# Kernel tuning notes

Hardware: AMD Instinct MI355X
Metric: run time of the kernel (lower is better)

## Reference

```python
import jax, jax.numpy as jnp
import numpy as np

K_NEIGH = 20
GROUPS = 4
KPTS = 9  # 3x3 deformable kernel
FH, FW = 240, 320


def _bn(x, p):
    # p: (4,C) rows = gamma, beta, running_mean, running_var ; x: (B,C,...)
    g, b, m, v = p[0], p[1], p[2], p[3]
    shp = (1, -1) + (1,) * (x.ndim - 2)
    return (x - m.reshape(shp)) * (g.reshape(shp) / jnp.sqrt(v.reshape(shp) + 1e-5)) + b.reshape(shp)


def _lrelu(x):
    return jnp.where(x >= 0, x, 0.2 * x)


def _c1x1(x, w):  # w: (Cout,Cin)
    return jnp.einsum('oc,bc...->bo...', w, x)


def _hswish(x):
    return x * jnp.clip(x + 3.0, 0.0, 6.0) / 6.0


def _coord_att(x, c1w, c1b, bnp, chw, chb, cww, cwb):
    B, C, H, W = x.shape
    ph = x.mean(axis=3, keepdims=True)                              # (B,C,H,1)
    pw = x.mean(axis=2, keepdims=True).transpose(0, 1, 3, 2)        # (B,C,W,1)
    y = jnp.concatenate([ph, pw], axis=2)                           # (B,C,H+W,1)
    y = _hswish(_bn(_c1x1(y, c1w) + c1b.reshape(1, -1, 1, 1), bnp))
    yh, yw = y[:, :, :H], y[:, :, H:]
    ah = jax.nn.sigmoid(_c1x1(yh, chw) + chb.reshape(1, -1, 1, 1))                         # (B,C,H,1)
    aw = jax.nn.sigmoid(_c1x1(yw.transpose(0, 1, 3, 2), cww) + cwb.reshape(1, -1, 1, 1))   # (B,C,1,W)
    return x * ah * aw


def _knn(x, k):
    xx = jnp.sum(x * x, axis=1)                     # (B,N)
    inner = jnp.einsum('bcn,bcm->bnm', x, x)
    pd = 2.0 * inner - xx[:, :, None] - xx[:, None, :]   # negative sq. distance
    return jax.lax.top_k(pd, k)[1]                  # (B,N,k)


def _graph_feature(x, k):
    B, C, N = x.shape
    idx = _knn(x, k)
    xt = x.transpose(0, 2, 1)                       # (B,N,C)
    nb = jax.vmap(lambda a, i: a[i])(xt, idx)       # (B,N,k,C)
    ctr = xt[:, :, None, :]
    f = jnp.concatenate([nb - ctr, jnp.broadcast_to(ctr, (B, N, k, C))], axis=3)
    return f.transpose(0, 3, 1, 2)                  # (B,2C,N,k)


def _dcnv4(x, off_w, off_b, val_w, val_b, out_w, out_b):
    B, C, H, W = x.shape
    Cg = C // GROUPS
    xh = x.transpose(0, 2, 3, 1)                    # (B,H,W,C)
    value = xh @ val_w + val_b
    om = (xh @ off_w + off_b).reshape(B, H, W, GROUPS, KPTS, 3)
    offs, mask = om[..., :2], om[..., 2]            # DCNv4: mask used un-normalized
    ky, kx = jnp.meshgrid(jnp.arange(-1, 2), jnp.arange(-1, 2), indexing='ij')
    kgrid = jnp.stack([kx.ravel(), ky.ravel()], -1).astype(x.dtype)      # (K,2) xy
    gy, gx = jnp.meshgrid(jnp.arange(H), jnp.arange(W), indexing='ij')
    base = jnp.stack([gx, gy], -1).astype(x.dtype)  # (H,W,2)
    loc = base[None, :, :, None, None, :] + kgrid + offs                 # (B,H,W,G,K,2)
    vflat = value.reshape(B, H * W, GROUPS, Cg)
    outs = []
    for g in range(GROUPS):
        lx = loc[:, :, :, g, :, 0]
        ly = loc[:, :, :, g, :, 1]                  # (B,H,W,K)
        x0 = jnp.floor(lx); y0 = jnp.floor(ly)
        wx = lx - x0; wy = ly - y0
        vg = vflat[:, :, g]                         # (B,HW,Cg)
        samp = jnp.zeros((B, H, W, KPTS, Cg), x.dtype)
        for yi, xi, w in ((y0, x0, (1 - wx) * (1 - wy)), (y0, x0 + 1, wx * (1 - wy)),
                          (y0 + 1, x0, (1 - wx) * wy), (y0 + 1, x0 + 1, wx * wy)):
            inb = (yi >= 0) & (yi < H) & (xi >= 0) & (xi < W)
            ii = (jnp.clip(yi, 0, H - 1) * W + jnp.clip(xi, 0, W - 1)).astype(jnp.int32)
            gathered = jax.vmap(lambda v, i: v[i])(vg, ii.reshape(B, -1)).reshape(B, H, W, KPTS, Cg)
            samp = samp + (w * inb)[..., None] * gathered
        outs.append(jnp.einsum('bhwk,bhwkc->bhwc', mask[:, :, :, g], samp))
    out = jnp.concatenate(outs, axis=-1) @ out_w + out_b
    return out.transpose(0, 3, 1, 2)


def setup_inputs() -> dict:
    key = jax.random.key(0)
    ks = jax.random.split(key, 24)
    B, N, IN_CH, FEAT_DIM = 2, 4096, 3, 128
    pc = jax.random.normal(ks[0], (B, 8, N), jnp.float32)
    v = jax.random.uniform(ks[1], (B, 1, N), jnp.float32, -240.0, 240.0)
    u = jax.random.uniform(ks[2], (B, 1, N), jnp.float32, -320.0, 320.0)
    pc = jnp.concatenate([v, u, pc[:, 2:]], axis=1)
    feat_s00 = jax.random.normal(ks[3], (B, IN_CH, 480, 640), jnp.float32)

    def w(k, shape, s=0.05):
        return jax.random.normal(k, shape, jnp.float32) * s

    def bn(c):
        return jnp.stack([jnp.ones(c), jnp.zeros(c), jnp.zeros(c), jnp.ones(c)]).astype(jnp.float32)

    OC = GROUPS * KPTS * 3
    return dict(
        pc_xyzrgb=pc, feat_s00=feat_s00,
        preconv_w=w(ks[4], (24, IN_CH, 3, 3)), preconv_b=jnp.zeros(24, jnp.float32),
        ca_c1_w=w(ks[5], (8, 24)), ca_c1_b=jnp.zeros(8, jnp.float32), ca_bn=bn(8),
        ca_ch_w=w(ks[6], (24, 8)), ca_ch_b=jnp.zeros(24, jnp.float32),
        ca_cw_w=w(ks[7], (24, 8)), ca_cw_b=jnp.zeros(24, jnp.float32),
        conv1_w=w(ks[8], (64, 64)), bn1=bn(64),
        conv2_w=w(ks[9], (64, 128)), bn2=bn(64),
        conv3_w=w(ks[10], (128, 128)), bn3=bn(128),
        lin4a_w=w(ks[11], (256, 256)), lin4b_w=w(ks[12], (256, 64)),
        dcn5_off_w=w(ks[13], (64, OC), 0.01), dcn5_off_b=jnp.zeros(OC, jnp.float32),
        dcn5_val_w=w(ks[14], (64, 64)), dcn5_val_b=jnp.zeros(64, jnp.float32),
        dcn5_out_w=w(ks[15], (64, 64)), dcn5_out_b=jnp.zeros(64, jnp.float32), bn5=bn(64),
        dcn6_off_w=w(ks[16], (64, OC), 0.01), dcn6_off_b=jnp.zeros(OC, jnp.float32),
        dcn6_val_w=w(ks[17], (64, 64)), dcn6_val_b=jnp.zeros(64, jnp.float32),
        dcn6_out_w=w(ks[18], (64, 64)), dcn6_out_b=jnp.zeros(64, jnp.float32), bn6=bn(64),
        conv7a_w=w(ks[19], (64, 64)), conv7b_w=w(ks[20], (FEAT_DIM, 64)),
    )


def reference(pc_xyzrgb, feat_s00, preconv_w, preconv_b, ca_c1_w, ca_c1_b, ca_bn, ca_ch_w, ca_ch_b,
              ca_cw_w, ca_cw_b, conv1_w, bn1, conv2_w, bn2, conv3_w, bn3, lin4a_w, lin4b_w,
              dcn5_off_w, dcn5_off_b, dcn5_val_w, dcn5_val_b, dcn5_out_w, dcn5_out_b, bn5,
              dcn6_off_w, dcn6_off_b, dcn6_val_w, dcn6_val_b, dcn6_out_w, dcn6_out_b, bn6,
              conv7a_w, conv7b_w):
    B, _, N = pc_xyzrgb.shape
    v = jnp.floor(pc_xyzrgb[:, 0] + 240.0).astype(jnp.int32).reshape(-1)
    u = jnp.floor(pc_xyzrgb[:, 1] + 320.0).astype(jnp.int32).reshape(-1)
    bi = jnp.repeat(jnp.arange(B, dtype=jnp.int32), N)
    # preConv: 3x3 conv + CoordAtt, then gather per-point 2D features
    fs1 = jax.lax.conv_general_dilated(feat_s00, preconv_w, (1, 1), 'SAME') + preconv_b.reshape(1, -1, 1, 1)
    fs1 = _coord_att(fs1, ca_c1_w, ca_c1_b, ca_bn, ca_ch_w, ca_ch_b, ca_cw_w, ca_cw_b)
    fs1 = fs1.transpose(0, 2, 3, 1)                                  # (B,480,640,24)
    feat_2d = fs1[bi, v, u].reshape(B, N, 24)
    feat_3d = jnp.concatenate([pc_xyzrgb.transpose(0, 2, 1), feat_2d], axis=2).transpose(0, 2, 1)  # (B,32,N)
    x = _lrelu(_bn(_c1x1(_graph_feature(feat_3d, K_NEIGH), conv1_w), bn1))
    x1 = x.max(axis=-1)                                              # (B,64,N)
    x = _lrelu(_bn(_c1x1(_graph_feature(x1, K_NEIGH), conv2_w), bn2))
    x2 = x.max(axis=-1)
    x = _lrelu(_bn(_c1x1(_graph_feature(x2, K_NEIGH), conv3_w), bn3))
    x3 = x.max(axis=-1)                                              # (B,128,N)
    x = jnp.concatenate([x1, x2, x3], axis=1).transpose(0, 2, 1)     # (B,N,256)
    x = (x @ lin4a_w) @ lin4b_w                                      # (B,N,64)
    fm = jnp.zeros((B, FH, FW, 64), x.dtype).at[bi, v // 2, u // 2].add(x.reshape(B * N, 64))
    fm = jax.nn.softmax(fm.transpose(0, 3, 1, 2), axis=1)            # (B,64,240,320)
    fm = _lrelu(_bn(_dcnv4(fm, dcn5_off_w, dcn5_off_b, dcn5_val_w, dcn5_val_b, dcn5_out_w, dcn5_out_b), bn5))
    fm = _lrelu(_bn(_dcnv4(fm, dcn6_off_w, dcn6_off_b, dcn6_val_w, dcn6_val_b, dcn6_out_w, dcn6_out_b), bn6))
    fm = _c1x1(_c1x1(fm, conv7a_w), conv7b_w)                        # (B,feat_dim,240,320)
    idx1 = jnp.stack([bi, v // 2, u // 2], axis=0)
    return fm, idx1
```

## Files before the change

kernel.cpp:

```cpp
#include <hip/hip_runtime.h>
#include <math.h>

#define B_    2
#define N_    4096
#define BN_   (B_*N_)
#define H0    480
#define W0    640
#define FH_   240
#define FW_   320
#define PIX_  (B_*FH_*FW_)
#define KNN_K 20

static const size_t OFF_RS   = 0;
static const size_t OFF_CS   = 2944;
static const size_t OFF_PH   = 6784;
static const size_t OFF_PW   = 29824;
static const size_t OFF_Y8   = 60544;
static const size_t OFF_AH   = 78464;
static const size_t OFF_AW   = 101504;
static const size_t OFF_VB   = 132224;
static const size_t OFF_UB   = 140416;
static const size_t OFF_F3D  = 148608;
static const size_t OFF_XX   = 410752;
static const size_t OFF_IDX  = 5661824;
static const size_t OFF_X1   = 5825664;
static const size_t OFF_X2   = 6349952;
static const size_t OFF_X3   = 6874240;
static const size_t OFF_T1   = 7922816;
static const size_t OFF_T2   = 7926912;
static const size_t OFF_T3   = 7935104;
static const size_t OFF_T7A  = 7951488;
static const size_t OFF_T7B  = 7955584;
static const size_t OFF_FMA  = 7963776;
static const size_t OFF_FMV  = 17794176;
static const size_t OFF_FMB  = 27624576;

__global__ void k_transpose(const float* __restrict__ w1, const float* __restrict__ w2,
                            const float* __restrict__ w3, const float* __restrict__ w7a,
                            const float* __restrict__ w7b,
                            float* __restrict__ t1, float* __restrict__ t2,
                            float* __restrict__ t3, float* __restrict__ t7a,
                            float* __restrict__ t7b) {
    int t = blockIdx.x * 256 + threadIdx.x;
    if (t < 4096) {
        int i = t >> 6, o = t & 63; t1[i*64+o] = w1[o*64+i];
    } else if (t < 12288) {
        int r = t - 4096; int i = r >> 6, o = r & 63; t2[i*64+o] = w2[o*128+i];
    } else if (t < 28672) {
        int r = t - 12288; int i = r >> 7, o = r & 127; t3[i*128+o] = w3[o*128+i];
    } else if (t < 32768) {
        int r = t - 28672; int c = r >> 6, o = r & 63; t7a[c*64+o] = w7a[o*64+c];
    } else if (t < 40960) {
        int r = t - 32768; int o = r >> 7, p = r & 127; t7b[o*128+p] = w7b[p*64+o];
    }
}

__global__ void k_colsum(const float* __restrict__ img, float* __restrict__ cs) {
    int bc = blockIdx.x; int x = threadIdx.x;
    const float* p = img + (size_t)bc * H0 * W0;
    float acc = 0.f;
    for (int h = 0; h < H0; ++h) acc += p[h * W0 + x];
    cs[bc * W0 + x] = acc;
}
__global__ void k_rowsum(const float* __restrict__ img, float* __restrict__ rs) {
    int bc = blockIdx.x; int y = threadIdx.x;
    const float* p = img + (size_t)bc * H0 * W0 + (size_t)y * W0;
    float acc = 0.f;
    for (int x = 0; x < W0; ++x) acc += p[x];
    rs[bc * H0 + y] = acc;
}

__global__ void k_ph(const float* __restrict__ img, const float* __restrict__ rs,
                     const float* __restrict__ w, const float* __restrict__ bias,
                     float* __restrict__ ph) {
    int t = blockIdx.x * 256 + threadIdx.x;
    if (t >= B_ * 24 * H0) return;
    int h = t % H0; int bc = t / H0; int c = bc % 24; int b = bc / 24;
    float acc = 0.f;
    for (int ic = 0; ic < 3; ++ic)
        for (int dy = 0; dy < 3; ++dy) {
            int y = h + dy - 1;
            if ((unsigned)y >= (unsigned)H0) continue;
            float r = rs[(b*3+ic)*H0 + y];
            const float* row = img + (size_t)((b*3+ic)*H0 + y) * W0;
            float e0 = row[0], eL = row[W0-1];
            const float* wp = w + ((c*3+ic)*3+dy)*3;
            acc += wp[0]*(r - eL) + wp[1]*r + wp[2]*(r - e0);
        }
    ph[t] = bias[c] + acc / 640.0f;
}
__global__ void k_pw(const float* __restrict__ img, const float* __restrict__ cs,
                     const float* __restrict__ w, const float* __restrict__ bias,
                     float* __restrict__ pw) {
    int t = blockIdx.x * 256 + threadIdx.x;
    if (t >= B_ * 24 * W0) return;
    int x = t % W0; int bc = t / W0; int c = bc % 24; int b = bc / 24;
    float acc = 0.f;
    for (int ic = 0; ic < 3; ++ic)
        for (int dx = 0; dx < 3; ++dx) {
            int xx = x + dx - 1;
            if ((unsigned)xx >= (unsigned)W0) continue;
            float csv = cs[(b*3+ic)*W0 + xx];
            const float* base = img + (size_t)(b*3+ic) * H0 * W0;
            float top = base[xx];
            float bot = base[(size_t)(H0-1)*W0 + xx];
            const float* wp = w + ((c*3+ic)*3)*3 + dx;
            acc += wp[0]*(csv - bot) + wp[3]*csv + wp[6]*(csv - top);
        }
    pw[t] = bias[c] + acc / 480.0f;
}

__global__ void k_y8(const float* __restrict__ ph, const float* __restrict__ pw,
                     const float* __restrict__ c1w, const float* __restrict__ c1b,
                     const float* __restrict__ bnp, float* __restrict__ y8) {
    int t = blockIdx.x * 256 + threadIdx.x;
    if (t >= B_ * 8 * 1120) return;
    int pos = t % 1120; int bj = t / 1120; int j = bj % 8; int b = bj / 8;
    float s = c1b[j];
    for (int c = 0; c < 24; ++c) {
        float yv = (pos < H0) ? ph[(b*24+c)*H0 + pos] : pw[(b*24+c)*W0 + (pos - H0)];
        s = fmaf(c1w[j*24+c], yv, s);
    }
    float g = bnp[j], be = bnp[8+j], m = bnp[16+j], va = bnp[24+j];
    float v = (s - m) * (g / sqrtf(va + 1e-5f)) + be;
    float hs = v * fminf(fmaxf(v + 3.f, 0.f), 6.f) * (1.f/6.f);
    y8[(b*8+j)*1120 + pos] = hs;
}
__global__ void k_ahw(const float* __restrict__ y8,
                      const float* __restrict__ chw, const float* __restrict__ chb,
                      const float* __restrict__ cww, const float* __restrict__ cwb,
                      float* __restrict__ ah, float* __restrict__ aw) {
    int t = blockIdx.x * 256 + threadIdx.x;
    if (t >= B_ * 24 * 1120) return;
    int pos = t % 1120; int bc = t / 1120; int c = bc % 24; int b = bc / 24;
    if (pos < H0) {
        float s = chb[c];
        for (int j = 0; j < 8; ++j) s = fmaf(chw[c*8+j], y8[(b*8+j)*1120 + pos], s);
        ah[(b*24+c)*H0 + pos] = 1.f / (1.f + expf(-s));
    } else {
        float s = cwb[c];
        for (int j = 0; j < 8; ++j) s = fmaf(cww[c*8+j], y8[(b*8+j)*1120 + pos], s);
        aw[(b*24+c)*W0 + (pos - H0)] = 1.f / (1.f + expf(-s));
    }
}

__global__ void k_feat3d(const float* __restrict__ pc, const float* __restrict__ img,
                         const float* __restrict__ w, const float* __restrict__ bias,
                         const float* __restrict__ ah, const float* __restrict__ aw,
                         float* __restrict__ f3d, int* __restrict__ vbuf,
                         int* __restrict__ ubuf, float* __restrict__ idx_out) {
    int t = blockIdx.x * 256 + threadIdx.x;
    if (t >= BN_ * 32) return;
    int c = t & 31; int bn = t >> 5; int b = bn >> 12; int n = bn & (N_-1);
    float pv = pc[(b*8 + 0)*N_ + n];
    float pu = pc[(b*8 + 1)*N_ + n];
    int v = (int)floorf(pv + 240.f);
    int u = (int)floorf(pu + 320.f);
    float f;
    if (c < 8) {
        f = pc[(b*8 + c)*N_ + n];
    } else {
        int co = c - 8;
        float acc = bias[co];
        for (int ic = 0; ic < 3; ++ic)
            for (int dy = 0; dy < 3; ++dy) {
                int y = v + dy - 1;
                if ((unsigned)y >= (unsigned)H0) continue;
                for (int dx = 0; dx < 3; ++dx) {
                    int x = u + dx - 1;
                    if ((unsigned)x >= (unsigned)W0) continue;
                    acc = fmaf(w[((co*3+ic)*3+dy)*3+dx],
                               img[((size_t)(b*3+ic)*H0 + y)*W0 + x], acc);
                }
            }
        f = acc * ah[(b*24+co)*H0 + v] * aw[(b*24+co)*W0 + u];
    }
    f3d[(size_t)bn*32 + c] = f;
    if (c == 0) {
        vbuf[bn] = v; ubuf[bn] = u;
        idx_out[bn] = (float)b;
        idx_out[BN_ + bn] = (float)(v >> 1);
        idx_out[2*BN_ + bn] = (float)(u >> 1);
    }
}

template<int C>
__global__ void k_sqnorm(const float* __restrict__ X, float* __restrict__ XX) {
    int t = blockIdx.x * 256 + threadIdx.x;
    if (t >= BN_) return;
    float acc = 0.f;
    const float* p = X + (size_t)t * C;
#pragma unroll
    for (int i = 0; i < C; ++i) acc = fmaf(p[i], p[i], acc);
    XX[t] = acc;
}

template<int C>
__launch_bounds__(256, 2)
__global__ void k_dist(const float* __restrict__ X, const float* __restrict__ XX,
                       float* __restrict__ pd, int b) {
    __shared__ float As[C*128];
    __shared__ float Bs[C*128];
    int tid = threadIdx.x;
    int t = blockIdx.x;
    int I = (int)((-1.0f + sqrtf(1.0f + 8.0f*(float)t)) * 0.5f);
    while ((I*(I+1))/2 > t) --I;
    while (((I+1)*(I+2))/2 <= t) ++I;
    int J = t - (I*(I+1))/2;
    {
        int r = tid >> 1, c0 = (tid & 1) * (C/2);
        const float* qa = X + ((size_t)(b*N_ + I*128 + r)) * C + c0;
        const float* ca = X + ((size_t)(b*N_ + J*128 + r)) * C + c0;
#pragma unroll
        for (int m = 0; m < C/8; ++m) {
            float4 va = *(const float4*)(qa + m*4);
            float4 vb = *(const float4*)(ca + m*4);
            int c = c0 + m*4;
            As[(c+0)*128+r]=va.x; As[(c+1)*128+r]=va.y; As[(c+2)*128+r]=va.z; As[(c+3)*128+r]=va.w;
            Bs[(c+0)*128+r]=vb.x; Bs[(c+1)*128+r]=vb.y; Bs[(c+2)*128+r]=vb.z; Bs[(c+3)*128+r]=vb.w;
        }
    }
    __syncthreads();
    int tx = tid & 15, ty = tid >> 4;
    float acc[8][8];
#pragma unroll
    for (int i=0;i<8;++i)
#pragma unroll
        for (int j=0;j<8;++j) acc[i][j]=0.f;
    for (int k = 0; k < C; ++k) {
        float4 a0 = *(const float4*)&As[k*128 + ty*8];
        float4 a1 = *(const float4*)&As[k*128 + ty*8 + 4];
        float4 b0 = *(const float4*)&Bs[k*128 + tx*8];
        float4 b1 = *(const float4*)&Bs[k*128 + tx*8 + 4];
        float av[8] = {a0.x,a0.y,a0.z,a0.w,a1.x,a1.y,a1.z,a1.w};
        float bv[8] = {b0.x,b0.y,b0.z,b0.w,b1.x,b1.y,b1.z,b1.w};
#pragma unroll
        for (int i = 0; i < 8; ++i)
#pragma unroll
            for (int j = 0; j < 8; ++j)
                acc[i][j] = fmaf(av[i], bv[j], acc[i][j]);
    }
    float xq[8], xc[8];
#pragma unroll
    for (int i = 0; i < 8; ++i) {
        xq[i] = XX[b*N_ + I*128 + ty*8 + i];
        xc[i] = XX[b*N_ + J*128 + tx*8 + i];
    }
#pragma unroll
    for (int i = 0; i < 8; ++i) {
        int row = I*128 + ty*8 + i;
        float4 o0, o1;
        o0.x = 2.f*acc[i][0] - xq[i] - xc[0]; o0.y = 2.f*acc[i][1] - xq[i] - xc[1];
        o0.z = 2.f*acc[i][2] - xq[i] - xc[2]; o0.w = 2.f*acc[i][3] - xq[i] - xc[3];
        o1.x = 2.f*acc[i][4] - xq[i] - xc[4]; o1.y = 2.f*acc[i][5] - xq[i] - xc[5];
        o1.z = 2.f*acc[i][6] - xq[i] - xc[6]; o1.w = 2.f*acc[i][7] - xq[i] - xc[7];
        *(float4*)&pd[(size_t)row*N_ + J*128 + tx*8]     = o0;
        *(float4*)&pd[(size_t)row*N_ + J*128 + tx*8 + 4] = o1;
    }
    if (I != J) {
#pragma unroll
        for (int j = 0; j < 8; ++j) {
            int row = J*128 + tx*8 + j;
            float4 m0, m1;
            m0.x = 2.f*acc[0][j] - xc[j] - xq[0]; m0.y = 2.f*acc[1][j] - xc[j] - xq[1];
            m0.z = 2.f*acc[2][j] - xc[j] - xq[2]; m0.w = 2.f*acc[3][j] - xc[j] - xq[3];
            m1.x = 2.f*acc[4][j] - xc[j] - xq[4]; m1.y = 2.f*acc[5][j] - xc[j] - xq[5];
            m1.z = 2.f*acc[6][j] - xc[j] - xq[6]; m1.w = 2.f*acc[7][j] - xc[j] - xq[7];
            *(float4*)&pd[(size_t)row*N_ + I*128 + ty*8]     = m0;
            *(float4*)&pd[(size_t)row*N_ + I*128 + ty*8 + 4] = m1;
        }
    }
}

__launch_bounds__(256)
__global__ void k_select(const float* __restrict__ pd, int* __restrict__ idxb, int b) {
    int wv = threadIdx.x >> 6, lane = threadIdx.x & 63;
    int q = blockIdx.x * 4 + wv;
    const float* row = pd + (size_t)q * N_;
    float val[12]; int idx[12];
#pragma unroll
    for (int j = 0; j < 12; ++j) { val[j] = -INFINITY; idx[j] = 0x7fffffff; }
    for (int t = 0; t < N_ / 256; ++t) {
        float4 v4 = *(const float4*)(row + t * 256 + lane * 4);
        float vv[4] = {v4.x, v4.y, v4.z, v4.w};
#pragma unroll
        for (int j = 0; j < 4; ++j) {
            float v = vv[j];
            if (v > val[11]) {
                float cv = v; int cc = t * 256 + lane * 4 + j; bool ins = false;
#pragma unroll
                for (int s = 0; s < 12; ++s) {
                    bool sw = ins || (cv > val[s]);
                    if (sw) {
                        float tv = val[s]; val[s] = cv; cv = tv;
                        int ti = idx[s]; idx[s] = cc; cc = ti;
                        ins = true;
                    }
                }
            }
        }
    }
    int nb = 0;
    float hv = val[0]; int hi = idx[0];
#pragma unroll 1
    for (int slot = 0; slot < KNN_K; ++slot) {
        float wvv = hv; int wi = hi; int wl = lane;
#pragma unroll
        for (int off = 1; off < 64; off <<= 1) {
            float ov = __shfl_xor(wvv, off);
            int   oi = __shfl_xor(wi, off);
            int   ol = __shfl_xor(wl, off);
            bool take = (ov > wvv) || (ov == wvv && oi < wi);
            if (take) { wvv = ov; wi = oi; wl = ol; }
        }
        if (lane == slot) nb = wi;
        bool pop = (lane == wl);
#pragma unroll
        for (int s = 0; s < 11; ++s)
            if (pop) { val[s] = val[s+1]; idx[s] = idx[s+1]; }
        if (pop) { val[11] = -INFINITY; idx[11] = 0x7fffffff; }
        hv = val[0]; hi = idx[0];
    }
    if (lane < KNN_K) idxb[(size_t)(b * N_ + q) * KNN_K + lane] = nb;
}

template<int CIN, int COUT, int P>
__launch_bounds__(256, 2)
__global__ void edgeconv(const float* __restrict__ X, const int* __restrict__ idxb,
                         const float* __restrict__ wT, const float* __restrict__ bnp,
                         float* __restrict__ Y) {
    __shared__ float sctr[P][CIN];
    __shared__ float snb[P][KNN_K * CIN];
    int base = blockIdx.x * P;
    int tid = threadIdx.x;
    const int CIN4 = CIN / 4;
    if (tid < P * CIN4) {
        int p = tid / CIN4, i4 = tid % CIN4;
        ((float4*)sctr[p])[i4] = ((const float4*)&X[(size_t)(base + p) * CIN])[i4];
    }
    for (int j = tid; j < P * KNN_K * CIN4; j += 256) {
        int r = j / CIN4, i4 = j % CIN4;
        int p = r / KNN_K, k = r % KNN_K;
        int b = (base + p) / N_;
        int ni = idxb[(size_t)(base + p) * KNN_K + k];
        ((float4*)snb[p])[k * CIN4 + i4] =
            ((const float4*)&X[((size_t)b * N_ + ni) * CIN])[i4];
    }
    __syncthreads();
    int p = tid / COUT, o = tid % COUT;
    float wreg[CIN];
#pragma unroll
    for (int i = 0; i < CIN; ++i) wreg[i] = wT[i * COUT + o];
    float g = bnp[o], bb = bnp[COUT + o], m = bnp[2*COUT + o], va = bnp[3*COUT + o];
    float a = g / sqrtf(va + 1e-5f);
    float sh = bb - m * a;
    float accc = 0.f;
#pragma unroll
    for (int i = 0; i < CIN; ++i)
        accc = fmaf(wT[(CIN + i) * COUT + o] - wreg[i], sctr[p][i], accc);
    float mx = -INFINITY;
    for (int k = 0; k < KNN_K; ++k) {
        const float4* nb4 = (const float4*)&snb[p][k * CIN];
        float s = accc;
#pragma unroll
        for (int i4 = 0; i4 < CIN4; ++i4) {
            float4 v = nb4[i4];
            s = fmaf(wreg[4*i4+0], v.x, s);
            s = fmaf(wreg[4*i4+1], v.y, s);
            s = fmaf(wreg[4*i4+2], v.z, s);
            s = fmaf(wreg[4*i4+3], v.w, s);
        }
        float r = fmaf(s, a, sh);
        r = (r >= 0.f) ? r : 0.2f * r;
        mx = fmaxf(mx, r);
    }
    Y[(size_t)(base + p) * COUT + o] = mx;
}

__launch_bounds__(256)
__global__ void k_lin4(const float* __restrict__ x1, const float* __restrict__ x2,
                       const float* __restrict__ x3, const float* __restrict__ l4a,
                       const float* __restrict__ l4b, const int* __restrict__ vbuf,
                       const int* __restrict__ ubuf, float* __restrict__ fmA) {
    int p0 = blockIdx.x * 4; int tid = threadIdx.x;
    __shared__ float xc[4][256]; __shared__ float t1s[4][256];
    for (int j = tid; j < 1024; j += 256) {
        int p = j >> 8, i = j & 255;
        int bn = p0 + p;
        float v;
        if (i < 64)       v = x1[(size_t)bn*64 + i];
        else if (i < 128) v = x2[(size_t)bn*64 + i - 64];
        else              v = x3[(size_t)bn*128 + i - 128];
        xc[p][i] = v;
    }
    __syncthreads();
    float acc[4] = {0.f, 0.f, 0.f, 0.f};
#pragma unroll 8
    for (int i = 0; i < 256; ++i) {
        float wv = l4a[i*256 + tid];
#pragma unroll
        for (int p = 0; p < 4; ++p) acc[p] = fmaf(xc[p][i], wv, acc[p]);
    }
#pragma unroll
    for (int p = 0; p < 4; ++p) t1s[p][tid] = acc[p];
    __syncthreads();
    int o = tid & 63, pg = tid >> 6;
    float a2 = 0.f;
#pragma unroll 8
    for (int i = 0; i < 256; ++i) a2 = fmaf(t1s[pg][i], l4b[i*64 + o], a2);
    int bn = p0 + pg;
    int b = bn >> 12; int v = vbuf[bn] >> 1; int u = ubuf[bn] >> 1;
    atomicAdd(fmA + ((size_t)(b*FH_ + v)*FW_ + u)*64 + o, a2);
}

__launch_bounds__(256)
__global__ void k_dcnval(const float* __restrict__ in, const float* __restrict__ vw,
                         const float* __restrict__ vb, float* __restrict__ val,
                         float* __restrict__ smout, int do_sm) {
    __shared__ float sx[8][64];
    int tid = threadIdx.x;
    size_t base = (size_t)blockIdx.x * 512;
    if (tid < 128) ((float4*)sx)[tid] = *((const float4*)(in + base) + tid);
    __syncthreads();
    int o = tid & 63; int pg = tid >> 6;
    if (do_sm) {
        float x0 = sx[pg][o], x1 = sx[pg+4][o];
        float m0 = x0, m1 = x1;
        for (int off = 32; off > 0; off >>= 1) {
            m0 = fmaxf(m0, __shfl_xor(m0, off));
            m1 = fmaxf(m1, __shfl_xor(m1, off));
        }
        float e0 = expf(x0 - m0), e1 = expf(x1 - m1);
        float s0 = e0, s1 = e1;
        for (int off = 32; off > 0; off >>= 1) {
            s0 += __shfl_xor(s0, off);
            s1 += __shfl_xor(s1, off);
        }
        float r0 = e0 / s0, r1 = e1 / s1;
        smout[base + (size_t)pg*64 + o]     = r0;
        smout[base + (size_t)(pg+4)*64 + o] = r1;
        sx[pg][o] = r0; sx[pg+4][o] = r1;
        __syncthreads();
    }
    float bias = vb[o];
    float a0 = 0.f, a1 = 0.f;
#pragma unroll
    for (int i4 = 0; i4 < 16; ++i4) {
        float4 x0 = *(const float4*)&sx[pg][i4*4];
        float4 x1 = *(const float4*)&sx[pg+4][i4*4];
        float w0 = vw[(i4*4+0)*64 + o], w1 = vw[(i4*4+1)*64 + o];
        float w2 = vw[(i4*4+2)*64 + o], w3 = vw[(i4*4+3)*64 + o];
        a0 = fmaf(x0.x,w0,a0); a0 = fmaf(x0.y,w1,a0); a0 = fmaf(x0.z,w2,a0); a0 = fmaf(x0.w,w3,a0);
        a1 = fmaf(x1.x,w0,a1); a1 = fmaf(x1.y,w1,a1); a1 = fmaf(x1.z,w2,a1); a1 = fmaf(x1.w,w3,a1);
    }
    val[base + (size_t)pg*64 + o]     = a0 + bias;
    val[base + (size_t)(pg+4)*64 + o] = a1 + bias;
}

__launch_bounds__(256, 5)
__global__ void k_dcn64(const float* __restrict__ in, const float* __restrict__ val,
                        const float* __restrict__ ow, const float* __restrict__ ob,
                        const float* __restrict__ pwm, const float* __restrict__ pbm,
                        const float* __restrict__ bnp, float* __restrict__ out) {
    __shared__ float xT[64*36];
    __shared__ float somU[64*68];
    __shared__ float stapA[4][40][8];
    int tid = threadIdx.x;
    int blk = blockIdx.x;
    int b = blk / 2400;
    int hw0 = (blk % 2400) * 32;
    size_t pix0 = (size_t)b * (FH_*FW_) + hw0;

    {
        int px = tid >> 3, c0 = (tid & 7) * 8;
        const float* ip = in + (pix0 + px) * 64 + c0;
#pragma unroll
        for (int m = 0; m < 2; ++m) {
            float4 v = *(const float4*)(ip + m*4);
            int c = c0 + m*4;
            xT[(c+0)*36 + px] = v.x; xT[(c+1)*36 + px] = v.y;
            xT[(c+2)*36 + px] = v.z; xT[(c+3)*36 + px] = v.w;
        }
    }
    __builtin_amdgcn_wave_barrier();

    {
        int tx = tid & 15, ty = tid >> 4;
        int oadr[7];
#pragma unroll
        for (int j = 0; j < 7; ++j) {
            int o = tx + 16*j;
            oadr[j] = (o < 108) ? o : 107;
        }
        float acc[2][7];
#pragma unroll
        for (int i=0;i<2;++i)
#pragma unroll
            for (int j=0;j<7;++j) acc[i][j]=0.f;
        for (int c = 0; c < 64; ++c) {
            float2 a = *(const float2*)&xT[c*36 + ty*2];
            const float* owc = ow + c*108;
            float bv[7];
#pragma unroll
            for (int j = 0; j < 7; ++j) bv[j] = owc[oadr[j]];
#pragma unroll
            for (int j = 0; j < 7; ++j) {
                acc[0][j] = fmaf(a.x, bv[j], acc[0][j]);
                acc[1][j] = fmaf(a.y, bv[j], acc[1][j]);
            }
        }
#pragma unroll
        for (int j = 0; j < 7; ++j) {
            int o = tx + 16*j;
            if (o < 108) {
                float bias = ob[o];
                somU[(ty*2+0)*113 + o] = acc[0][j] + bias;
                somU[(ty*2+1)*113 + o] = acc[1][j] + bias;
            }
        }
    }
    __builtin_amdgcn_wave_barrier();

    int wv = tid >> 6, lane = tid & 63;
    const float* vb0 = val + (size_t)b * (FH_*FW_) * 64;
    int lane4 = lane << 2;
    for (int j = 0; j < 8; ++j) {
        int px = wv*8 + j;
        if (lane < 36) {
            int g = lane / 9, k = lane % 9;
            int hw = hw0 + px;
            int h = hw / FW_, w = hw % FW_;
            float lx = (float)(w + (k%3) - 1) + somU[px*113 + g*27 + k*3 + 0];
            float ly = (float)(h + (k/3) - 1) + somU[px*113 + g*27 + k*3 + 1];
            float msk = somU[px*113 + g*27 + k*3 + 2];
            float x0f = floorf(lx), y0f = floorf(ly);
            float wx = lx - x0f, wy = ly - y0f;
            int x0 = (int)x0f, y0 = (int)y0f;
            bool xi0 = (unsigned)x0 < (unsigned)FW_, xi1 = (unsigned)(x0+1) < (unsigned)FW_;
            bool yi0 = (unsigned)y0 < (unsigned)FH_, yi1 = (unsigned)(y0+1) < (unsigned)FH_;
            int x0c = min(max(x0, 0), FW_-1), x1c = min(max(x0+1, 0), FW_-1);
            int y0c = min(max(y0, 0), FH_-1), y1c = min(max(y0+1, 0), FH_-1);
            float4 fA, fW;
            fA.x = __int_as_float((y0c*FW_ + x0c) << 8);
            fA.y = __int_as_float((y0c*FW_ + x1c) << 8);
            fA.z = __int_as_float((y1c*FW_ + x0c) << 8);
            fA.w = __int_as_float((y1c*FW_ + x1c) << 8);
            fW.x = (xi0 && yi0) ? msk*(1.f-wx)*(1.f-wy) : 0.f;
            fW.y = (xi1 && yi0) ? msk*wx*(1.f-wy)       : 0.f;
            fW.z = (xi0 && yi1) ? msk*(1.f-wx)*wy       : 0.f;
            fW.w = (xi1 && yi1) ? msk*wx*wy             : 0.f;
            *(float4*)&stapA[wv][lane][0] = fA;
            *(float4*)&stapA[wv][lane][4] = fW;
        }
        __builtin_amdgcn_wave_barrier();
        {
            int g9 = (lane >> 4) * 9;
            float acc0 = 0.f, acc1 = 0.f;
#pragma unroll
            for (int k = 0; k < 9; ++k) {
                float4 A = *(const float4*)&stapA[wv][g9 + k][0];
                float4 W = *(const float4*)&stapA[wv][g9 + k][4];
                int a00 = __float_as_int(A.x) + lane4;
                int a01 = __float_as_int(A.y) + lane4;
                int a10 = __float_as_int(A.z) + lane4;
                int a11 = __float_as_int(A.w) + lane4;
                float v00 = *(const float*)((const char*)vb0 + (unsigned)a00);
                float v01 = *(const float*)((const char*)vb0 + (unsigned)a01);
                float v10 = *(const float*)((const char*)vb0 + (unsigned)a10);
                float v11 = *(const float*)((const char*)vb0 + (unsigned)a11);
                acc0 = fmaf(W.x, v00, acc0);
                acc1 = fmaf(W.y, v01, acc1);
                acc0 = fmaf(W.z, v10, acc0);
                acc1 = fmaf(W.w, v11, acc1);
            }
            xT[lane*36 + px] = acc0 + acc1;
        }
        __builtin_amdgcn_wave_barrier();
    }

    __syncthreads();
    for (int m = 0; m < 4; ++m) {
        int idx = tid + 256*m;
        int c = idx >> 4, o4 = (idx & 15) * 4;
        float4 v = *(const float4*)(pwm + c*64 + o4);
        *(float4*)&somU[c*68 + o4] = v;
    }
    __syncthreads();

    {
        int tx = tid & 15, ty = tid >> 4;
        float acc[2][4];
#pragma unroll
        for (int i=0;i<2;++i)
#pragma unroll
            for (int j=0;j<4;++j) acc[i][j]=0.f;
        for (int c = 0; c < 64; ++c) {
            float2 a = *(const float2*)&xT[c*36 + ty*2];
            float4 bb = *(const float4*)&somU[c*68 + tx*4];
            acc[0][0] = fmaf(a.x, bb.x, acc[0][0]);
            acc[0][1] = fmaf(a.x, bb.y, acc[0][1]);
            acc[0][2] = fmaf(a.x, bb.z, acc[0][2]);
            acc[0][3] = fmaf(a.x, bb.w, acc[0][3]);
            acc[1][0] = fmaf(a.y, bb.x, acc[1][0]);
            acc[1][1] = fmaf(a.y, bb.y, acc[1][1]);
            acc[1][2] = fmaf(a.y, bb.z, acc[1][2]);
            acc[1][3] = fmaf(a.y, bb.w, acc[1][3]);
        }
#pragma unroll
        for (int i = 0; i < 2; ++i) {
            int px = ty*2 + i;
            float vr[4];
#pragma unroll
            for (int jj = 0; jj < 4; ++jj) {
                int o = tx*4 + jj;
                float aa = acc[i][jj] + pbm[o];
                float g = bnp[o], be = bnp[64+o], m = bnp[128+o], va = bnp[192+o];
                float sc = g / sqrtf(va + 1e-5f);
                float r = (aa - m) * sc + be;
                vr[jj] = (r >= 0.f) ? r : 0.2f * r;
            }
            *(float4*)&out[(pix0 + px)*64 + tx*4] = make_float4(vr[0],vr[1],vr[2],vr[3]);
        }
    }
}

__launch_bounds__(256)
__global__ void k_conv7(const float* __restrict__ in, const float* __restrict__ w7aT,
                        const float* __restrict__ w7bT, float* __restrict__ out) {
    int blk = blockIdx.x;
    int b = blk / ((FH_*FW_)/16);
    int hw0 = (blk % ((FH_*FW_)/16)) * 16;
    int tid = threadIdx.x;
    __shared__ float sx[16][64];
    __shared__ float st[16][64];
    for (int j = tid; j < 1024; j += 256) {
        int p = j >> 6, c = j & 63;
        sx[p][c] = in[((size_t)(b*(FH_*FW_) + hw0 + p))*64 + c];
    }
    __syncthreads();
    {
        int o = tid & 63, p4 = tid >> 6;
        float acc[4] = {0.f, 0.f, 0.f, 0.f};
#pragma unroll 8
        for (int c = 0; c < 64; ++c) {
            float wv = w7aT[c*64 + o];
#pragma unroll
            for (int j = 0; j < 4; ++j) acc[j] = fmaf(sx[p4*4+j][c], wv, acc[j]);
        }
#pragma unroll
        for (int j = 0; j < 4; ++j) st[p4*4+j][o] = acc[j];
    }
    __syncthreads();
    {
        int po = tid >> 1, half = tid & 1;
        float acc[8] = {0.f};
#pragma unroll 8
        for (int c = 0; c < 64; ++c) {
            float wv = w7bT[c*128 + po];
#pragma unroll
            for (int j = 0; j < 8; ++j) acc[j] = fmaf(st[half*8+j][c], wv, acc[j]);
        }
        float* op = out + ((size_t)b*128 + po)*(FH_*FW_) + hw0 + half*8;
        *(float4*)op       = make_float4(acc[0], acc[1], acc[2], acc[3]);
        *(float4*)(op + 4) = make_float4(acc[4], acc[5], acc[6], acc[7]);
    }
}

extern "C" void kernel_launch(void* const* d_in, const int* in_sizes, int n_in,
                              void* d_out, int out_size, void* d_ws, size_t ws_size,
                              hipStream_t stream) {
    (void)in_sizes; (void)n_in; (void)out_size; (void)ws_size;
    const float* pc   = (const float*)d_in[0];
    const float* img  = (const float*)d_in[1];
    const float* pcw  = (const float*)d_in[2];
    const float* pcb  = (const float*)d_in[3];
    const float* c1w  = (const float*)d_in[4];
    const float* c1b  = (const float*)d_in[5];
    const float* cabn = (const float*)d_in[6];
    const float* chw  = (const float*)d_in[7];
    const float* chb  = (const float*)d_in[8];
    const float* cww  = (const float*)d_in[9];
    const float* cwb  = (const float*)d_in[10];
    const float* w1   = (const float*)d_in[11];
    const float* bn1  = (const float*)d_in[12];
    const float* w2   = (const float*)d_in[13];
    const float* bn2  = (const float*)d_in[14];
    const float* w3   = (const float*)d_in[15];
    const float* bn3  = (const float*)d_in[16];
    const float* l4a  = (const float*)d_in[17];
    const float* l4b  = (const float*)d_in[18];
    const float* d5ow = (const float*)d_in[19];
    const float* d5ob = (const float*)d_in[20];
    const float* d5vw = (const float*)d_in[21];
    const float* d5vb = (const float*)d_in[22];
    const float* d5pw = (const float*)d_in[23];
    const float* d5pb = (const float*)d_in[24];
    const float* bn5  = (const float*)d_in[25];
    const float* d6ow = (const float*)d_in[26];
    const float* d6ob = (const float*)d_in[27];
    const float* d6vw = (const float*)d_in[28];
    const float* d6vb = (const float*)d_in[29];
    const float* d6pw = (const float*)d_in[30];
    const float* d6pb = (const float*)d_in[31];
    const float* bn6  = (const float*)d_in[32];
    const float* w7a  = (const float*)d_in[33];
    const float* w7b  = (const float*)d_in[34];

    float* ws  = (float*)d_ws;
    float* out = (float*)d_out;

    float* rs  = ws + OFF_RS;   float* cs  = ws + OFF_CS;
    float* ph  = ws + OFF_PH;   float* pw  = ws + OFF_PW;
    float* y8  = ws + OFF_Y8;   float* ah  = ws + OFF_AH;  float* aw = ws + OFF_AW;
    int*   vb  = (int*)(ws + OFF_VB);
    int*   ub  = (int*)(ws + OFF_UB);
    float* f3d = ws + OFF_F3D;  float* xx  = ws + OFF_XX;
    int*   idxb = (int*)(ws + OFF_IDX);
    float* x1  = ws + OFF_X1;   float* x2  = ws + OFF_X2;  float* x3 = ws + OFF_X3;
    float* t1  = ws + OFF_T1;   float* t2  = ws + OFF_T2;  float* t3 = ws + OFF_T3;
    float* t7a = ws + OFF_T7A;  float* t7b = ws + OFF_T7B;
    float* fmA = ws + OFF_FMA;  float* fmV = ws + OFF_FMV; float* fmB = ws + OFF_FMB;
    float* pdb = ws + OFF_FMA;

    k_transpose<<<160, 256, 0, stream>>>(w1, w2, w3, w7a, w7b, t1, t2, t3, t7a, t7b);
    k_colsum<<<B_*3, W0, 0, stream>>>(img, cs);
    k_rowsum<<<B_*3, H0, 0, stream>>>(img, rs);
    k_ph<<<(B_*24*H0 + 255)/256, 256, 0, stream>>>(img, rs, pcw, pcb, ph);
    k_pw<<<(B_*24*W0 + 255)/256, 256, 0, stream>>>(img, cs, pcw, pcb, pw);
    k_y8<<<(B_*8*1120 + 255)/256, 256, 0, stream>>>(ph, pw, c1w, c1b, cabn, y8);
    k_ahw<<<(B_*24*1120 + 255)/256, 256, 0, stream>>>(y8, chw, chb, cww, cwb, ah, aw);
    k_feat3d<<<(BN_*32)/256, 256, 0, stream>>>(pc, img, pcw, pcb, ah, aw, f3d, vb, ub,
                                               out + (size_t)B_*128*FH_*FW_);

    k_sqnorm<32><<<BN_/256, 256, 0, stream>>>(f3d, xx);
    for (int b = 0; b < B_; ++b) {
        k_dist<32><<<528, 256, 0, stream>>>(f3d, xx, pdb, b);
        k_select<<<N_/4, 256, 0, stream>>>(pdb, idxb, b);
    }
    edgeconv<32,64,4><<<BN_/4, 256, 0, stream>>>(f3d, idxb, t1, bn1, x1);
    k_sqnorm<64><<<BN_/256, 256, 0, stream>>>(x1, xx);
    for (int b = 0; b < B_; ++b) {
        k_dist<64><<<528, 256, 0, stream>>>(x1, xx, pdb, b);
        k_select<<<N_/4, 256, 0, stream>>>(pdb, idxb, b);
    }
    edgeconv<64,64,4><<<BN_/4, 256, 0, stream>>>(x1, idxb, t2, bn2, x2);
    k_sqnorm<64><<<BN_/256, 256, 0, stream>>>(x2, xx);
    for (int b = 0; b < B_; ++b) {
        k_dist<64><<<528, 256, 0, stream>>>(x2, xx, pdb, b);
        k_select<<<N_/4, 256, 0, stream>>>(pdb, idxb, b);
    }
    edgeconv<64,128,2><<<BN_/2, 256, 0, stream>>>(x2, idxb, t3, bn3, x3);

    hipMemsetAsync(fmA, 0, (size_t)PIX_ * 64 * sizeof(float), stream);
    k_lin4<<<BN_/4, 256, 0, stream>>>(x1, x2, x3, l4a, l4b, vb, ub, fmA);

    k_dcnval<<<PIX_/8, 256, 0, stream>>>(fmA, d5vw, d5vb, fmV, fmA, 1);
    k_dcn64<<<PIX_/32, 256, 0, stream>>>(fmA, fmV, d5ow, d5ob, d5pw, d5pb, bn5, fmB);
    k_dcnval<<<PIX_/8, 256, 0, stream>>>(fmB, d6vw, d6vb, fmV, fmB, 0);
    k_dcn64<<<PIX_/32, 256, 0, stream>>>(fmB, fmV, d6ow, d6ob, d6pw, d6pb, bn6, fmA);

    k_conv7<<<PIX_/16, 256, 0, stream>>>(fmA, t7a, t7b, out);
}
```

Before: 1.722 ms.

## Fuse coordinate-attention prologue kernels and compute squared norms inside distance tiles

Merges the row/column-sum, ph/pw and y8/attention kernels into three fused launches, keeping the 8-channel intermediate in registers instead of a workspace buffer. It also drops the separate squared-norm kernels and computes each tile's point norms from the shared-memory operands inside k_dist. This removes several small launches and a global round-trip for the norms. The cost is that the norms are recomputed for every tile pair, the k_y8ahw grid is now only 9 blocks, and k_dist gains an extra barrier.

```diff
diff --git a/kernel.cpp b/kernel.cpp
--- a/kernel.cpp
+++ b/kernel.cpp
@@ -55,92 +55,106 @@
     }
 }
 
-__global__ void k_colsum(const float* __restrict__ img, float* __restrict__ cs) {
-    int bc = blockIdx.x; int x = threadIdx.x;
-    const float* p = img + (size_t)bc * H0 * W0;
-    float acc = 0.f;
-    for (int h = 0; h < H0; ++h) acc += p[h * W0 + x];
-    cs[bc * W0 + x] = acc;
-}
-__global__ void k_rowsum(const float* __restrict__ img, float* __restrict__ rs) {
-    int bc = blockIdx.x; int y = threadIdx.x;
-    const float* p = img + (size_t)bc * H0 * W0 + (size_t)y * W0;
-    float acc = 0.f;
-    for (int x = 0; x < W0; ++x) acc += p[x];
-    rs[bc * H0 + y] = acc;
-}
-
-__global__ void k_ph(const float* __restrict__ img, const float* __restrict__ rs,
-                     const float* __restrict__ w, const float* __restrict__ bias,
-                     float* __restrict__ ph) {
+__global__ void k_sums(const float* __restrict__ img, float* __restrict__ cs,
+                       float* __restrict__ rs) {
     int t = blockIdx.x * 256 + threadIdx.x;
-    if (t >= B_ * 24 * H0) return;
-    int h = t % H0; int bc = t / H0; int c = bc % 24; int b = bc / 24;
-    float acc = 0.f;
-    for (int ic = 0; ic < 3; ++ic)
-        for (int dy = 0; dy < 3; ++dy) {
-            int y = h + dy - 1;
-            if ((unsigned)y >= (unsigned)H0) continue;
-            float r = rs[(b*3+ic)*H0 + y];
-            const float* row = img + (size_t)((b*3+ic)*H0 + y) * W0;
-            float e0 = row[0], eL = row[W0-1];
-            const float* wp = w + ((c*3+ic)*3+dy)*3;
-            acc += wp[0]*(r - eL) + wp[1]*r + wp[2]*(r - e0);
-        }
-    ph[t] = bias[c] + acc / 640.0f;
-}
-__global__ void k_pw(const float* __restrict__ img, const float* __restrict__ cs,
-                     const float* __restrict__ w, const float* __restrict__ bias,
-                     float* __restrict__ pw) {
+    if (t < 6*W0) {
+        int bc = t / W0, x = t % W0;
+        const float* p = img + (size_t)bc * H0 * W0;
+        float acc = 0.f;
+        for (int h = 0; h < H0; ++h) acc += p[h * W0 + x];
+        cs[bc * W0 + x] = acc;
+    } else {
+        int t2 = t - 6*W0;
+        if (t2 < 6*H0) {
+            int bc = t2 / H0, y = t2 % H0;
+            const float* p = img + (size_t)bc * H0 * W0 + (size_t)y * W0;
+            float acc = 0.f;
+            for (int x = 0; x < W0; ++x) acc += p[x];
+            rs[bc * H0 + y] = acc;
+        }
+    }
+}
+
+__global__ void k_phpw(const float* __restrict__ img, const float* __restrict__ rs,
+                       const float* __restrict__ cs, const float* __restrict__ w,
+                       const float* __restrict__ bias,
+                       float* __restrict__ ph, float* __restrict__ pw) {
     int t = blockIdx.x * 256 + threadIdx.x;
-    if (t >= B_ * 24 * W0) return;
-    int x = t % W0; int bc = t / W0; int c = bc % 24; int b = bc / 24;
-    float acc = 0.f;
-    for (int ic = 0; ic < 3; ++ic)
-        for (int dx = 0; dx < 3; ++dx) {
-            int xx = x + dx - 1;
-            if ((unsigned)xx >= (unsigned)W0) continue;
-            float csv = cs[(b*3+ic)*W0 + xx];
-            const float* base = img + (size_t)(b*3+ic) * H0 * W0;
-            float top = base[xx];
-            float bot = base[(size_t)(H0-1)*W0 + xx];
-            const float* wp = w + ((c*3+ic)*3)*3 + dx;
-            acc += wp[0]*(csv - bot) + wp[3]*csv + wp[6]*(csv - top);
-        }
-    pw[t] = bias[c] + acc / 480.0f;
-}
-
-__global__ void k_y8(const float* __restrict__ ph, const float* __restrict__ pw,
-                     const float* __restrict__ c1w, const float* __restrict__ c1b,
-                     const float* __restrict__ bnp, float* __restrict__ y8) {
+    if (t < B_ * 24 * H0) {
+        int h = t % H0; int bc = t / H0; int c = bc % 24; int b = bc / 24;
+        float acc = 0.f;
+        for (int ic = 0; ic < 3; ++ic)
+            for (int dy = 0; dy < 3; ++dy) {
+                int y = h + dy - 1;
+                if ((unsigned)y >= (unsigned)H0) continue;
+                float r = rs[(b*3+ic)*H0 + y];
+                const float* row = img + (size_t)((b*3+ic)*H0 + y) * W0;
+                float e0 = row[0], eL = row[W0-1];
+                const float* wp = w + ((c*3+ic)*3+dy)*3;
+                acc += wp[0]*(r - eL) + wp[1]*r + wp[2]*(r - e0);
+            }
+        ph[t] = bias[c] + acc / 640.0f;
+    } else {
+        int t2 = t - B_ * 24 * H0;
+        if (t2 < B_ * 24 * W0) {
+            int x = t2 % W0; int bc = t2 / W0; int c = bc % 24; int b = bc / 24;
+            float acc = 0.f;
+            for (int ic = 0; ic < 3; ++ic)
+                for (int dx = 0; dx < 3; ++dx) {
+                    int xx = x + dx - 1;
+                    if ((unsigned)xx >= (unsigned)W0) continue;
+                    float csv = cs[(b*3+ic)*W0 + xx];
+                    const float* base = img + (size_t)(b*3+ic) * H0 * W0;
+                    float top = base[xx];
+                    float bot = base[(size_t)(H0-1)*W0 + xx];
+                    const float* wp = w + ((c*3+ic)*3)*3 + dx;
+                    acc += wp[0]*(csv - bot) + wp[3]*csv + wp[6]*(csv - top);
+                }
+            pw[t2] = bias[c] + acc / 480.0f;
+        }
+    }
+}
+
+__global__ void k_y8ahw(const float* __restrict__ ph, const float* __restrict__ pw,
+                        const float* __restrict__ c1w, const float* __restrict__ c1b,
+                        const float* __restrict__ bnp,
+                        const float* __restrict__ chw, const float* __restrict__ chb,
+                        const float* __restrict__ cww, const float* __restrict__ cwb,
+                        float* __restrict__ ah, float* __restrict__ aw) {
     int t = blockIdx.x * 256 + threadIdx.x;
-    if (t >= B_ * 8 * 1120) return;
-    int pos = t % 1120; int bj = t / 1120; int j = bj % 8; int b = bj / 8;
-    float s = c1b[j];
-    for (int c = 0; c < 24; ++c) {
-        float yv = (pos < H0) ? ph[(b*24+c)*H0 + pos] : pw[(b*24+c)*W0 + (pos - H0)];
-        s = fmaf(c1w[j*24+c], yv, s);
-    }
-    float g = bnp[j], be = bnp[8+j], m = bnp[16+j], va = bnp[24+j];
-    float v = (s - m) * (g / sqrtf(va + 1e-5f)) + be;
-    float hs = v * fminf(fmaxf(v + 3.f, 0.f), 6.f) * (1.f/6.f);
-    y8[(b*8+j)*1120 + pos] = hs;
-}
-__global__ void k_ahw(const float* __restrict__ y8,
-                      const float* __restrict__ chw, const float* __restrict__ chb,
-                      const float* __restrict__ cww, const float* __restrict__ cwb,
-                      float* __restrict__ ah, float* __restrict__ aw) {
-    int t = blockIdx.x * 256 + threadIdx.x;
-    if (t >= B_ * 24 * 1120) return;
-    int pos = t % 1120; int bc = t / 1120; int c = bc % 24; int b = bc / 24;
+    if (t >= B_ * 1120) return;
+    int pos = t % 1120; int b = t / 1120;
+    float yv[24];
+#pragma unroll
+    for (int c = 0; c < 24; ++c)
+        yv[c] = (pos < H0) ? ph[(b*24+c)*H0 + pos] : pw[(b*24+c)*W0 + (pos - H0)];
+    float y8j[8];
+#pragma unroll
+    for (int j = 0; j < 8; ++j) {
+        float s = c1b[j];
+#pragma unroll
+        for (int c = 0; c < 24; ++c) s = fmaf(c1w[j*24+c], yv[c], s);
+        float g = bnp[j], be = bnp[8+j], m = bnp[16+j], va = bnp[24+j];
+        float v = (s - m) * (g / sqrtf(va + 1e-5f)) + be;
+        y8j[j] = v * fminf(fmaxf(v + 3.f, 0.f), 6.f) * (1.f/6.f);
+    }
     if (pos < H0) {
-        float s = chb[c];
-        for (int j = 0; j < 8; ++j) s = fmaf(chw[c*8+j], y8[(b*8+j)*1120 + pos], s);
-        ah[(b*24+c)*H0 + pos] = 1.f / (1.f + expf(-s));
+#pragma unroll
+        for (int c = 0; c < 24; ++c) {
+            float s = chb[c];
+#pragma unroll
+            for (int j = 0; j < 8; ++j) s = fmaf(chw[c*8+j], y8j[j], s);
+            ah[(b*24+c)*H0 + pos] = 1.f / (1.f + expf(-s));
+        }
     } else {
-        float s = cwb[c];
-        for (int j = 0; j < 8; ++j) s = fmaf(cww[c*8+j], y8[(b*8+j)*1120 + pos], s);
-        aw[(b*24+c)*W0 + (pos - H0)] = 1.f / (1.f + expf(-s));
+#pragma unroll
+        for (int c = 0; c < 24; ++c) {
+            float s = cwb[c];
+#pragma unroll
+            for (int j = 0; j < 8; ++j) s = fmaf(cww[c*8+j], y8j[j], s);
+            aw[(b*24+c)*W0 + (pos - H0)] = 1.f / (1.f + expf(-s));
+        }
     }
 }
 
@@ -185,22 +199,11 @@
 }
 
 template<int C>
-__global__ void k_sqnorm(const float* __restrict__ X, float* __restrict__ XX) {
-    int t = blockIdx.x * 256 + threadIdx.x;
-    if (t >= BN_) return;
-    float acc = 0.f;
-    const float* p = X + (size_t)t * C;
-#pragma unroll
-    for (int i = 0; i < C; ++i) acc = fmaf(p[i], p[i], acc);
-    XX[t] = acc;
-}
-
-template<int C>
 __launch_bounds__(256, 2)
-__global__ void k_dist(const float* __restrict__ X, const float* __restrict__ XX,
-                       float* __restrict__ pd, int b) {
+__global__ void k_dist(const float* __restrict__ X, float* __restrict__ pd, int b) {
     __shared__ float As[C*128];
     __shared__ float Bs[C*128];
+    __shared__ float sXX[256];
     int tid = threadIdx.x;
     int t = blockIdx.x;
     int I = (int)((-1.0f + sqrtf(1.0f + 8.0f*(float)t)) * 0.5f);
@@ -240,11 +243,28 @@
             for (int j = 0; j < 8; ++j)
                 acc[i][j] = fmaf(av[i], bv[j], acc[i][j]);
     }
+    {
+        float nacc = 0.f;
+        if (tid < 128) {
+            for (int c = 0; c < C; ++c) {
+                float v = As[c*128 + tid];
+                nacc = fmaf(v, v, nacc);
+            }
+        } else {
+            int r = tid - 128;
+            for (int c = 0; c < C; ++c) {
+                float v = Bs[c*128 + r];
+                nacc = fmaf(v, v, nacc);
+            }
+        }
+        sXX[tid] = nacc;
+    }
+    __syncthreads();
     float xq[8], xc[8];
 #pragma unroll
     for (int i = 0; i < 8; ++i) {
-        xq[i] = XX[b*N_ + I*128 + ty*8 + i];
-        xc[i] = XX[b*N_ + J*128 + tx*8 + i];
+        xq[i] = sXX[ty*8 + i];
+        xc[i] = sXX[128 + tx*8 + i];
     }
 #pragma unroll
     for (int i = 0; i < 8; ++i) {
@@ -711,10 +731,10 @@
 
     float* rs  = ws + OFF_RS;   float* cs  = ws + OFF_CS;
     float* ph  = ws + OFF_PH;   float* pw  = ws + OFF_PW;
-    float* y8  = ws + OFF_Y8;   float* ah  = ws + OFF_AH;  float* aw = ws + OFF_AW;
+    float* ah  = ws + OFF_AH;   float* aw  = ws + OFF_AW;
     int*   vb  = (int*)(ws + OFF_VB);
     int*   ub  = (int*)(ws + OFF_UB);
-    float* f3d = ws + OFF_F3D;  float* xx  = ws + OFF_XX;
+    float* f3d = ws + OFF_F3D;
     int*   idxb = (int*)(ws + OFF_IDX);
     float* x1  = ws + OFF_X1;   float* x2  = ws + OFF_X2;  float* x3 = ws + OFF_X3;
     float* t1  = ws + OFF_T1;   float* t2  = ws + OFF_T2;  float* t3 = ws + OFF_T3;
@@ -723,30 +743,24 @@
     float* pdb = ws + OFF_FMA;
 
     k_transpose<<<160, 256, 0, stream>>>(w1, w2, w3, w7a, w7b, t1, t2, t3, t7a, t7b);
-    k_colsum<<<B_*3, W0, 0, stream>>>(img, cs);
-    k_rowsum<<<B_*3, H0, 0, stream>>>(img, rs);
-    k_ph<<<(B_*24*H0 + 255)/256, 256, 0, stream>>>(img, rs, pcw, pcb, ph);
-    k_pw<<<(B_*24*W0 + 255)/256, 256, 0, stream>>>(img, cs, pcw, pcb, pw);
-    k_y8<<<(B_*8*1120 + 255)/256, 256, 0, stream>>>(ph, pw, c1w, c1b, cabn, y8);
-    k_ahw<<<(B_*24*1120 + 255)/256, 256, 0, stream>>>(y8, chw, chb, cww, cwb, ah, aw);
+    k_sums<<<27, 256, 0, stream>>>(img, cs, rs);
+    k_phpw<<<210, 256, 0, stream>>>(img, rs, cs, pcw, pcb, ph, pw);
+    k_y8ahw<<<9, 256, 0, stream>>>(ph, pw, c1w, c1b, cabn, chw, chb, cww, cwb, ah, aw);
     k_feat3d<<<(BN_*32)/256, 256, 0, stream>>>(pc, img, pcw, pcb, ah, aw, f3d, vb, ub,
                                                out + (size_t)B_*128*FH_*FW_);
 
-    k_sqnorm<32><<<BN_/256, 256, 0, stream>>>(f3d, xx);
     for (int b = 0; b < B_; ++b) {
-        k_dist<32><<<528, 256, 0, stream>>>(f3d, xx, pdb, b);
+        k_dist<32><<<528, 256, 0, stream>>>(f3d, pdb, b);
         k_select<<<N_/4, 256, 0, stream>>>(pdb, idxb, b);
     }
     edgeconv<32,64,4><<<BN_/4, 256, 0, stream>>>(f3d, idxb, t1, bn1, x1);
-    k_sqnorm<64><<<BN_/256, 256, 0, stream>>>(x1, xx);
     for (int b = 0; b < B_; ++b) {
-        k_dist<64><<<528, 256, 0, stream>>>(x1, xx, pdb, b);
+        k_dist<64><<<528, 256, 0, stream>>>(x1, pdb, b);
         k_select<<<N_/4, 256, 0, stream>>>(pdb, idxb, b);
     }
     edgeconv<64,64,4><<<BN_/4, 256, 0, stream>>>(x1, idxb, t2, bn2, x2);
-    k_sqnorm<64><<<BN_/256, 256, 0, stream>>>(x2, xx);
     for (int b = 0; b < B_; ++b) {
-        k_dist<64><<<528, 256, 0, stream>>>(x2, xx, pdb, b);
+        k_dist<64><<<528, 256, 0, stream>>>(x2, pdb, b);
         k_select<<<N_/4, 256, 0, stream>>>(pdb, idxb, b);
     }
     edgeconv<64,128,2><<<BN_/2, 256, 0, stream>>>(x2, idxb, t3, bn3, x3);
```

Result: no change. 1.692 ms (-1.8%).
